# Optimization experiments

Measured on AMD Instinct MI355X. Metric: run time of the kernel, lower is better.

Reference implementation:

```python
import jax, jax.numpy as jnp
import numpy as np

# dims: batch, seq, vocab, hidden, layers, heads, head_dim, intermediate
B, S, V, Hd, L, H, D, I = 2, 1024, 32000, 1024, 4, 16, 64, 4096
THETA = 1e6
EPS = 1e-6
TOPK = S // 2          # sparsity_ratio = 0.5 -> keep half of the keys per head
STD = 0.02
NEG = -1e9


def _ln(x, w, b):
    m = jnp.mean(x, -1, keepdims=True)
    v = jnp.mean((x - m) ** 2, -1, keepdims=True)
    return (x - m) * jax.lax.rsqrt(v + EPS) * w + b


def _rope_tables():
    inv = 1.0 / (THETA ** (np.arange(0, D, 2, dtype=np.float32) / D))
    f = np.arange(S, dtype=np.float32)[:, None] * inv[None, :]   # [S, D/2]
    emb = np.concatenate([f, f], -1)                              # [S, D]
    return jnp.asarray(np.cos(emb)), jnp.asarray(np.sin(emb))


def _rot(x):  # rotate-half, x: [B,H,S,D]
    x1, x2 = jnp.split(x, 2, axis=-1)
    return jnp.concatenate([-x2, x1], -1)


def setup_inputs() -> dict:
    key = jax.random.key(0)
    it = iter(jax.random.split(key, 24))
    p = lambda sh: jax.random.normal(next(it), sh, jnp.float32) * STD
    return {
        "input_ids": jax.random.randint(next(it), (B, S), 0, V, jnp.int32),
        "attention_mask": jnp.ones((B, S), jnp.float32),
        "embed": p((V, Hd)),
        "ln1_w": jnp.ones((L, Hd)), "ln1_b": jnp.zeros((L, Hd)),
        "Wq": p((L, Hd, Hd)), "Wk": p((L, Hd, Hd)),
        "Wv": p((L, Hd, Hd)), "Wo": p((L, Hd, Hd)),
        "Wr": p((L, Hd, H)),
        "ln2_w": jnp.ones((L, Hd)), "ln2_b": jnp.zeros((L, Hd)),
        "W1": p((L, Hd, I)), "b1": jnp.zeros((L, I)),
        "W2": p((L, I, Hd)), "b2": jnp.zeros((L, Hd)),
        "norm_w": jnp.ones((Hd,)), "norm_b": jnp.zeros((Hd,)),
        "lm_head": p((Hd, V)),
    }


def reference(input_ids, attention_mask, embed, ln1_w, ln1_b, Wq, Wk, Wv, Wo,
              Wr, ln2_w, ln2_b, W1, b1, W2, b2, norm_w, norm_b, lm_head):
    cos, sin = _rope_tables()                                   # [S, D]
    mask_add = (1.0 - attention_mask)[:, None, None, :] * NEG   # [B,1,1,S]
    x = embed[input_ids]                                        # [B,S,Hd]
    scale = 1.0 / np.sqrt(D)

    def block(x, p):
        h = _ln(x, p["ln1_w"], p["ln1_b"])
        heads = lambda w: jnp.einsum('bse,ed->bsd', h, w).reshape(B, S, H, D).transpose(0, 2, 1, 3)
        q, k, v = heads(p["Wq"]), heads(p["Wk"]), heads(p["Wv"])  # [B,H,S,D]
        q = q * cos + _rot(q) * sin
        k = k * cos + _rot(k) * sin
        router = jnp.einsum('bse,eh->bhs', h, p["Wr"])            # [B,H,S]
        kth = jax.lax.top_k(router, TOPK)[0][..., -1:]            # [B,H,1]
        bias = jnp.where(router >= kth, jax.nn.log_sigmoid(router), NEG)[:, :, None, :]
        logits = jnp.einsum('bhsd,bhtd->bhst', q, k) * scale + bias + mask_add
        attn = jax.nn.softmax(logits, -1)
        o = jnp.einsum('bhst,bhtd->bhsd', attn, v).transpose(0, 2, 1, 3).reshape(B, S, Hd)
        x = x + jnp.einsum('bse,ed->bsd', o, p["Wo"])
        h2 = _ln(x, p["ln2_w"], p["ln2_b"])
        m = jax.nn.silu(jnp.einsum('bse,ei->bsi', h2, p["W1"]) + p["b1"])
        x = x + jnp.einsum('bsi,ie->bse', m, p["W2"]) + p["b2"]
        return x, None

    layer_params = {"ln1_w": ln1_w, "ln1_b": ln1_b, "Wq": Wq, "Wk": Wk,
                    "Wv": Wv, "Wo": Wo, "Wr": Wr, "ln2_w": ln2_w,
                    "ln2_b": ln2_b, "W1": W1, "b1": b1, "W2": W2, "b2": b2}
    x, _ = jax.lax.scan(block, x, layer_params)
    x = _ln(x, norm_w, norm_b)
    return jnp.einsum('bse,ev->bsv', x, lm_head)   # [B,S,V]
```

## Files before the change

kernel.cpp:

```cpp
#include <hip/hip_runtime.h>
#include <hip/hip_bf16.h>

#define Bdim 2
#define Sdim 1024
#define Vdim 32000
#define HDdim 1024
#define Ldim 4
#define Hdim 16
#define Ddim 64
#define Idim 4096
#define BSdim 2048

typedef __attribute__((ext_vector_type(8))) short bf16x8;
typedef __attribute__((ext_vector_type(4))) float f32x4;

__device__ __forceinline__ unsigned short f2bf(float f) {
    __hip_bfloat16 h = __float2bfloat16(f);
    return *reinterpret_cast<unsigned short*>(&h);
}

#define MFMA16(a, b, c) __builtin_amdgcn_mfma_f32_16x16x32_bf16((a), (b), (c), 0, 0, 0)

#define GLD16(gp, lp)                                                            \
    __builtin_amdgcn_global_load_lds((const __attribute__((address_space(1))) void*)(gp), \
                                     (__attribute__((address_space(3))) void*)(lp), 16, 0, 0)

template <int N>
__device__ __forceinline__ void vwait() {
    if constexpr (N == 2) asm volatile("s_waitcnt vmcnt(2)" ::: "memory");
    else if constexpr (N == 3) asm volatile("s_waitcnt vmcnt(3)" ::: "memory");
    else if constexpr (N == 4) asm volatile("s_waitcnt vmcnt(4)" ::: "memory");
    else if constexpr (N == 6) asm volatile("s_waitcnt vmcnt(6)" ::: "memory");
}

__global__ __launch_bounds__(256) void tables_kernel(float* __restrict__ cosT, float* __restrict__ sinT) {
    int i = blockIdx.x * 256 + threadIdx.x;
    int d = i & 63;
    int s = i >> 6;
    float inv = powf(1.0e6f, -((float)(2 * (d & 31))) / 64.0f);
    float f = (float)s * inv;
    cosT[i] = cosf(f);
    sinT[i] = sinf(f);
}

__global__ __launch_bounds__(256) void embed_kernel(const int* __restrict__ ids, const float* __restrict__ emb,
                                                    float* __restrict__ x) {
    int m = blockIdx.x;
    int tid = threadIdx.x;
    int id = ids[m];
    const float4* src = (const float4*)(emb + (size_t)id * HDdim);
    ((float4*)(x + (size_t)m * HDdim))[tid] = src[tid];
}

__global__ __launch_bounds__(256) void ln_kernel(const float* __restrict__ x, const float* __restrict__ w,
                                                 const float* __restrict__ bw, unsigned short* __restrict__ outH,
                                                 const float* __restrict__ Wr, float* __restrict__ routerO) {
    int m = blockIdx.x;
    int tid = threadIdx.x;
    float4 a = ((const float4*)(x + (size_t)m * HDdim))[tid];
    float s = a.x + a.y + a.z + a.w;
    #pragma unroll
    for (int o = 1; o < 64; o <<= 1) s += __shfl_xor(s, o);
    __shared__ float red[4], red2[4];
    if ((tid & 63) == 0) red[tid >> 6] = s;
    __syncthreads();
    float mean = (red[0] + red[1] + red[2] + red[3]) * (1.0f / 1024.0f);
    float dx = a.x - mean, dy = a.y - mean, dz = a.z - mean, dw = a.w - mean;
    float s2 = dx * dx + dy * dy + dz * dz + dw * dw;
    #pragma unroll
    for (int o = 1; o < 64; o <<= 1) s2 += __shfl_xor(s2, o);
    if ((tid & 63) == 0) red2[tid >> 6] = s2;
    __syncthreads();
    float var = (red2[0] + red2[1] + red2[2] + red2[3]) * (1.0f / 1024.0f);
    float rs = rsqrtf(var + 1e-6f);
    float4 wv = ((const float4*)w)[tid];
    float4 bv = ((const float4*)bw)[tid];
    float v0 = dx * rs * wv.x + bv.x;
    float v1 = dy * rs * wv.y + bv.y;
    float v2 = dz * rs * wv.z + bv.z;
    float v3 = dw * rs * wv.w + bv.w;
    short4 st = make_short4((short)f2bf(v0), (short)f2bf(v1), (short)f2bf(v2), (short)f2bf(v3));
    *(short4*)(outH + (size_t)m * HDdim + tid * 4) = st;

    if (Wr) {
        __shared__ float rbuf[256][16];
        __shared__ float pbuf[16][17];
        float part[16];
        const float* wr0 = Wr + (size_t)(tid * 4) * Hdim;
        #pragma unroll
        for (int h = 0; h < 16; h++)
            part[h] = v0 * wr0[h] + v1 * wr0[16 + h] + v2 * wr0[32 + h] + v3 * wr0[48 + h];
        #pragma unroll
        for (int h4 = 0; h4 < 4; h4++)
            *(float4*)&rbuf[tid][h4 * 4] = make_float4(part[h4 * 4], part[h4 * 4 + 1], part[h4 * 4 + 2], part[h4 * 4 + 3]);
        __syncthreads();
        {
            int h = tid & 15, g = tid >> 4;
            float sgr = 0.0f;
            #pragma unroll
            for (int i = 0; i < 16; i++) sgr += rbuf[g * 16 + i][h];
            pbuf[g][h] = sgr;
        }
        __syncthreads();
        if (tid < 16) {
            float tot = 0.0f;
            #pragma unroll
            for (int g = 0; g < 16; g++) tot += pbuf[g][tid];
            int b = m >> 10, sI = m & 1023;
            routerO[((size_t)(b * Hdim + tid)) * Sdim + sI] = tot;
        }
    }
}

__global__ __launch_bounds__(1024) void topk_kernel(const float* __restrict__ router, const float* __restrict__ amask,
                                                    float* __restrict__ biasC, int* __restrict__ idxC,
                                                    int* __restrict__ ntA) {
    int bh = blockIdx.x;
    int t = threadIdx.x;
    __shared__ float r[1024];
    __shared__ float kths;
    __shared__ int wcnt[16];
    float v = router[(size_t)bh * Sdim + t];
    r[t] = v;
    __syncthreads();
    int gt = 0, eq = 0;
    for (int j = 0; j < 1024; j++) {
        float xv = r[j];
        gt += (xv > v) ? 1 : 0;
        eq += (xv == v) ? 1 : 0;
    }
    if (gt < 512 && gt + eq >= 512) kths = v;
    biasC[(size_t)bh * Sdim + t] = -1e9f;
    idxC[(size_t)bh * Sdim + t] = 0;
    __syncthreads();
    float kth = kths;
    bool sel = (v >= kth);
    unsigned long long m = __ballot(sel);
    int wid = t >> 6, lane = t & 63;
    if (lane == 0) wcnt[wid] = __popcll(m);
    __syncthreads();
    int base = 0;
    for (int w = 0; w < wid; w++) base += wcnt[w];
    if (sel) {
        int rank = base + (int)__popcll(m & ((1ull << lane) - 1ull));
        float bias = (v >= 0.0f) ? -log1pf(expf(-v)) : (v - log1pf(expf(v)));
        int b = bh >> 4;
        bias += (1.0f - amask[b * Sdim + t]) * (-1e9f);
        biasC[(size_t)bh * Sdim + rank] = bias;
        idxC[(size_t)bh * Sdim + rank] = t;
    }
    if (t == 0) {
        int tot = 0;
        #pragma unroll
        for (int w = 0; w < 16; w++) tot += wcnt[w];
        ntA[bh] = (tot + 63) >> 6;
    }
}

__global__ __launch_bounds__(256) void tconv_kernel(const float* __restrict__ S0,
                                                    unsigned short* __restrict__ D, int K, int ldS) {
    __shared__ float t[32][33];
    int kt = blockIdx.y * 32, nt = blockIdx.x * 32;
    int r = threadIdx.x >> 3, c4 = (threadIdx.x & 7) * 4;
    float4 v = *(const float4*)(S0 + (size_t)(kt + r) * ldS + nt + c4);
    t[r][c4] = v.x; t[r][c4 + 1] = v.y; t[r][c4 + 2] = v.z; t[r][c4 + 3] = v.w;
    __syncthreads();
    short4 o = make_short4((short)f2bf(t[c4][r]), (short)f2bf(t[c4 + 1][r]),
                           (short)f2bf(t[c4 + 2][r]), (short)f2bf(t[c4 + 3][r]));
    *(short4*)(D + (size_t)(nt + r) * K + kt + c4) = o;
}

__global__ __launch_bounds__(256) void tconv_all(const float* __restrict__ Wq, const float* __restrict__ Wk,
                                                 const float* __restrict__ Wv, const float* __restrict__ Wo,
                                                 const float* __restrict__ W1, const float* __restrict__ W2,
                                                 unsigned short* __restrict__ wtsL) {
    const size_t M1 = 1u << 20;
    int bid = blockIdx.x;
    int lid = bid / 12288, sub = bid - lid * 12288;
    unsigned short* wl = wtsL + (size_t)lid * 12 * M1;
    const float* S;
    unsigned short* D;
    int K, ldS, nt, kt;
    if (sub < 4096) {
        int z = sub >> 10, t = sub & 1023;
        S = ((z == 0) ? Wq : (z == 1) ? Wk : (z == 2) ? Wv : Wo) + (size_t)lid * M1;
        D = wl + (size_t)z * M1;
        K = 1024; ldS = 1024; nt = t & 31; kt = t >> 5;
    } else if (sub < 8192) {
        int t = sub - 4096;
        S = W1 + (size_t)lid * 4 * M1; D = wl + 4 * M1;
        K = 1024; ldS = 4096; nt = t % 128; kt = t / 128;
    } else {
        int t = sub - 8192;
        S = W2 + (size_t)lid * 4 * M1; D = wl + 8 * M1;
        K = 4096; ldS = 1024; nt = t % 32; kt = t / 32;
    }
    __shared__ float tb[32][33];
    int ktb = kt * 32, ntb = nt * 32;
    int r = threadIdx.x >> 3, c4 = (threadIdx.x & 7) * 4;
    float4 v = *(const float4*)(S + (size_t)(ktb + r) * ldS + ntb + c4);
    tb[r][c4] = v.x; tb[r][c4 + 1] = v.y; tb[r][c4 + 2] = v.z; tb[r][c4 + 3] = v.w;
    __syncthreads();
    short4 o = make_short4((short)f2bf(tb[c4][r]), (short)f2bf(tb[c4 + 1][r]),
                           (short)f2bf(tb[c4 + 2][r]), (short)f2bf(tb[c4 + 3][r]));
    *(short4*)(D + (size_t)(ntb + r) * K + ktb + c4) = o;
}

__global__ __launch_bounds__(256) void vgather_kernel(const unsigned short* __restrict__ v16,
                                                      const int* __restrict__ idxC, const int* __restrict__ ntA,
                                                      unsigned short* __restrict__ vTc) {
    int jt = blockIdx.x;
    int bh = blockIdx.y;
    if (jt >= ntA[bh]) return;
    __shared__ unsigned short T[64][72];
    int tid = threadIdx.x;
    int jl = tid >> 2;
    int part = tid & 3;
    int j = jt * 64 + jl;
    int src = idxC[(size_t)bh * Sdim + j];
    const unsigned short* vr = v16 + ((size_t)bh * Sdim + src) * Ddim + part * 16;
    *(bf16x8*)&T[jl][part * 16] = *(const bf16x8*)vr;
    *(bf16x8*)&T[jl][part * 16 + 8] = *(const bf16x8*)(vr + 8);
    __syncthreads();
    int d = tid >> 2;
    int xr = (d & 7) << 3;
    unsigned short* dst = vTc + ((size_t)bh * Ddim + d) * Sdim + jt * 64;
    #pragma unroll
    for (int cc = 0; cc < 2; cc++) {
        int tb = (tid & 3) * 16 + cc * 8;
        bf16x8 o;
        #pragma unroll
        for (int i = 0; i < 8; i++) o[i] = (short)T[tb + i][d];
        *(bf16x8*)(dst + (tb ^ xr)) = o;
    }
}

template <int EPI, int BM, int BN, int WM, int WN>
__global__ __launch_bounds__(512) void gemm8p(
    const unsigned short* __restrict__ A, const unsigned short* __restrict__ Bt,
    float* __restrict__ OF, unsigned short* __restrict__ Hq, unsigned short* __restrict__ Hk,
    unsigned short* __restrict__ Hv, const float* __restrict__ bias,
    const float* __restrict__ cosT, const float* __restrict__ sinT,
    int Kc, int ldK, int ldC, int gridM, int gridN) {
    constexpr int MI = BM / WM / 16, NI = BN / WN / 16;
    constexpr int MH = MI / 2, NH = NI / 2;
    constexpr int LA = BM / 128, LB = BN / 128;
    constexpr int HA = BM / WM / 2;
    constexpr int HB = BN / WN / 2;
    constexpr int ABUF = BM * 64, BBUF = BN * 64;

    __shared__ unsigned short lds[2 * ABUF + 2 * BBUF];

    int bid = blockIdx.x;
    const int nwg = gridDim.x;
    if ((nwg & 7) == 0) bid = (bid & 7) * (nwg >> 3) + (bid >> 3);
    const int mn = gridM * gridN;
    const int ks = bid / mn;
    const int rem = bid - ks * mn;
    const int bm = (rem % gridM) * BM;
    const int bn = (rem / gridM) * BN;
    const unsigned short* Ap = A + (size_t)ks * Kc;
    const unsigned short* Bp = Bt + (size_t)ks * Kc;

    const int tid = threadIdx.x;
    const int lane = tid & 63, wid = tid >> 6;
    const int lc = lane & 15, lg = lane >> 4;
    const int wwm = wid / WN, wwn = wid % WN;

    const int srow = tid >> 3;
    const int scol = ((tid & 7) ^ (srow & 7)) * 8;
    const int ak0 = (lg * 8) ^ ((lc & 7) * 8);
    const int ak1 = (32 + lg * 8) ^ ((lc & 7) * 8);

    f32x4 acc[MI][NI];
    f32x4 zero = {0.0f, 0.0f, 0.0f, 0.0f};
    #pragma unroll
    for (int i = 0; i < MI; i++)
        #pragma unroll
        for (int j = 0; j < NI; j++) acc[i][j] = zero;

    bf16x8 a[MH][2], b0[NH][2], b1[NH][2];

    auto stage_a = [&](int half, int nbuf, int kt) {
        #pragma unroll
        for (int j = 0; j < LA; j++) {
            const int idx = j * 64 + srow;
            const int grow = (idx / HA) * (BM / WM) + half * HA + (idx % HA);
            const unsigned short* g = Ap + (size_t)(bm + grow) * ldK + kt + scol;
            GLD16(g, &lds[nbuf * ABUF + half * (ABUF / 2) + (j * 512 + tid) * 8]);
        }
    };
    auto stage_b = [&](int half, int nbuf, int kt) {
        #pragma unroll
        for (int j = 0; j < LB; j++) {
            const int idx = j * 64 + srow;
            const int grow = (idx / HB) * (BN / WN) + half * HB + (idx % HB);
            const unsigned short* g = Bp + (size_t)(bn + grow) * ldK + kt + scol;
            GLD16(g, &lds[2 * ABUF + nbuf * BBUF + half * (BBUF / 2) + (j * 512 + tid) * 8]);
        }
    };

#define DS_A(mh_, cur_)                                                                   \
    _Pragma("unroll") for (int m = 0; m < MH; m++) {                                      \
        const int ro = (cur_)*ABUF + (mh_) * (ABUF / 2) + (wwm * HA + m * 16 + lc) * 64;  \
        a[m][0] = *(const bf16x8*)&lds[ro + ak0];                                         \
        a[m][1] = *(const bf16x8*)&lds[ro + ak1];                                         \
    }
#define DS_B(bb_, nh_, cur_)                                                              \
    _Pragma("unroll") for (int n = 0; n < NH; n++) {                                      \
        const int ro = 2 * ABUF + (cur_)*BBUF + (nh_) * (BBUF / 2) + (wwn * HB + n * 16 + lc) * 64; \
        bb_[n][0] = *(const bf16x8*)&lds[ro + ak0];                                       \
        bb_[n][1] = *(const bf16x8*)&lds[ro + ak1];                                       \
    }
#define MFMA_PH(mh_, nh_, bb_)                                                            \
    __builtin_amdgcn_s_setprio(1);                                                        \
    _Pragma("unroll") for (int m = 0; m < MH; m++) _Pragma("unroll") for (int n = 0; n < NH; n++) { \
        acc[(mh_)*MH + m][(nh_)*NH + n] = MFMA16(a[m][0], bb_[n][0], acc[(mh_)*MH + m][(nh_)*NH + n]); \
        acc[(mh_)*MH + m][(nh_)*NH + n] = MFMA16(a[m][1], bb_[n][1], acc[(mh_)*MH + m][(nh_)*NH + n]); \
    }                                                                                     \
    __builtin_amdgcn_s_setprio(0);
#define BAR_PRE()                                                                         \
    __builtin_amdgcn_sched_barrier(0);                                                    \
    __builtin_amdgcn_s_barrier();
#define BAR_END()                                                                         \
    asm volatile("" ::: "memory");                                                        \
    __builtin_amdgcn_s_barrier();                                                         \
    __builtin_amdgcn_sched_barrier(0);

    stage_a(0, 0, 0);
    stage_b(0, 0, 0);
    stage_b(1, 0, 0);
    stage_a(1, 0, 0);
    vwait<LA + LB>();
    BAR_END();

    const int NT = Kc >> 6;
    for (int t = 0; t < NT; t++) {
        const int cur = t & 1, nxt = cur ^ 1;
        const int ktn = (t + 1 < NT) ? (t + 1) * 64 : t * 64;
        DS_A(0, cur);
        DS_B(b0, 0, cur);
        stage_a(0, nxt, ktn);
        BAR_PRE();
        MFMA_PH(0, 0, b0);
        vwait<2 * LA>();
        BAR_END();
        DS_B(b1, 1, cur);
        stage_b(0, nxt, ktn);
        BAR_PRE();
        MFMA_PH(0, 1, b1);
        vwait<LA + LB>();
        BAR_END();
        DS_A(1, cur);
        stage_b(1, nxt, ktn);
        BAR_PRE();
        MFMA_PH(1, 1, b1);
        BAR_END();
        stage_a(1, nxt, ktn);
        BAR_PRE();
        MFMA_PH(1, 0, b0);
        vwait<LA + LB>();
        BAR_END();
    }
    asm volatile("s_waitcnt vmcnt(0)" ::: "memory");
#undef DS_A
#undef DS_B
#undef MFMA_PH
#undef BAR_PRE
#undef BAR_END

    #pragma unroll
    for (int i = 0; i < MI; i++) {
        if (EPI == 1) {
            const int colbase = bn + wwn * (BN / WN);
            const int zc = colbase >> 10;
            unsigned short* OH = (zc == 0) ? Hq : (zc == 1) ? Hk : Hv;
            const int hcol = (colbase >> 6) & 15;
            #pragma unroll
            for (int r = 0; r < 4; r++) {
                int row = bm + wwm * (BM / WM) + i * 16 + lg * 4 + r;
                int b = row >> 10, s = row & 1023;
                size_t base = ((size_t)(b * Hdim + hcol) * Sdim + s) << 6;
                if (zc == 2) {
                    #pragma unroll
                    for (int j = 0; j < 4; j++) OH[base + j * 16 + lc] = f2bf(acc[i][j][r]);
                } else {
                    #pragma unroll
                    for (int j = 0; j < 2; j++) {
                        int d = j * 16 + lc;
                        float x1 = acc[i][j][r];
                        float x2 = acc[i][j + 2][r];
                        float c = cosT[s * 64 + d];
                        float sn = sinT[s * 64 + d];
                        OH[base + d] = f2bf(x1 * c - x2 * sn);
                        OH[base + d + 32] = f2bf(x2 * c + x1 * sn);
                    }
                }
            }
        } else {
            #pragma unroll
            for (int r = 0; r < 4; r++) {
                int row = bm + wwm * (BM / WM) + i * 16 + lg * 4 + r;
                #pragma unroll
                for (int j = 0; j < NI; j++) {
                    int col = bn + wwn * (BN / WN) + j * 16 + lc;
                    float v = acc[i][j][r];
                    if (EPI == 3) {
                        float t = v + bias[col];
                        Hq[(size_t)row * ldC + col] = f2bf(t / (1.0f + expf(-t)));
                    } else if (EPI == 6) {
                        if (ks == 0 && bias != nullptr) v += bias[col];
                        unsafeAtomicAdd(&OF[(size_t)row * ldC + col], v);
                    } else {
                        OF[(size_t)row * ldC + col] = v;
                    }
                }
            }
        }
    }
}

__global__ __launch_bounds__(256) void attn_kernel(const unsigned short* __restrict__ q16,
                                                   const unsigned short* __restrict__ k16,
                                                   const unsigned short* __restrict__ vTc,
                                                   const int* __restrict__ idxC,
                                                   const float* __restrict__ biasC,
                                                   const int* __restrict__ ntA,
                                                   unsigned short* __restrict__ o16) {
    const int qb = blockIdx.x;
    const int bh = blockIdx.y;
    const int tid = threadIdx.x;
    const int w = tid >> 6, lane = tid & 63;
    const int lg = lane >> 4, lc = lane & 15;
    const int nt = ntA[bh];

    __shared__ unsigned short Ks[2][64 * 64];
    __shared__ unsigned short Vs[2][64 * 64];
    __shared__ unsigned short Pq[4][16][72];
    __shared__ float sbAll[1024];

    {
        const float4 bv = ((const float4*)(biasC + (size_t)bh * Sdim))[tid];
        *(float4*)&sbAll[tid * 4] = bv;
    }

    const int qrow = qb * 64 + w * 16 + lc;
    const unsigned short* qbase = q16 + ((size_t)bh * Sdim + qrow) * Ddim;
    bf16x8 qf[2];
    qf[0] = *(const bf16x8*)(qbase + lg * 8);
    qf[1] = *(const bf16x8*)(qbase + 32 + lg * 8);

    const int grow = tid >> 3;
    const int gc = (tid & 7) * 8;
    const int ksw = (grow & 7) << 3;
    const unsigned short* kbase = k16 + (size_t)bh * Sdim * Ddim;
    const int* ibase = idxC + (size_t)bh * Sdim;
    const unsigned short* vbase = vTc + (size_t)bh * Ddim * Sdim;

    auto stageK = [&](int buf, int t1) {
        int s0 = ibase[t1 + grow];
        int s1 = ibase[t1 + 32 + grow];
        GLD16(kbase + (size_t)s0 * Ddim + (gc ^ ksw), &Ks[buf][tid * 8]);
        GLD16(kbase + (size_t)s1 * Ddim + (gc ^ ksw), &Ks[buf][2048 + tid * 8]);
    };

    {
        stageK(0, 0);
        const unsigned short* vg = vbase + (size_t)grow * Sdim + gc;
        GLD16(vg, &Vs[0][tid * 8]);
        GLD16(vg + 32 * Sdim, &Vs[0][2048 + tid * 8]);
    }
    __syncthreads();

    float m_i = -1e30f, l_i = 0.0f;
    f32x4 ot[4];
    f32x4 zero = {0.0f, 0.0f, 0.0f, 0.0f};
    #pragma unroll
    for (int fd = 0; fd < 4; fd++) ot[fd] = zero;

    const int sw = (lc & 7) << 3;

    for (int tt = 0; tt < nt; tt++) {
        const int cur = tt & 1;
        if (tt > 0) {
            asm volatile("s_waitcnt vmcnt(0)" ::: "memory");
            __builtin_amdgcn_sched_barrier(0);
            __builtin_amdgcn_s_barrier();
        }
        if (tt < nt - 1) {
            const int t1 = (tt + 1) * 64;
            stageK(cur ^ 1, t1);
            const unsigned short* vg = vbase + (size_t)grow * Sdim + t1 + gc;
            GLD16(vg, &Vs[cur ^ 1][tid * 8]);
            GLD16(vg + 32 * Sdim, &Vs[cur ^ 1][2048 + tid * 8]);
        }

        f32x4 sf[4];
        #pragma unroll
        for (int f = 0; f < 4; f++) {
            const int trow = f * 16 + lc;
            f32x4 a = zero;
            #pragma unroll
            for (int ks = 0; ks < 2; ks++) {
                bf16x8 kfr = *(bf16x8*)&Ks[cur][trow * 64 + ((ks * 32 + lg * 8) ^ sw)];
                a = MFMA16(kfr, qf[ks], a);
            }
            sf[f] = a;
        }
        const int t0 = tt * 64;
        float tmax = -1e30f;
        #pragma unroll
        for (int f = 0; f < 4; f++)
            #pragma unroll
            for (int j = 0; j < 4; j++) {
                float v = sf[f][j] * 0.125f + sbAll[t0 + f * 16 + lg * 4 + j];
                sf[f][j] = v;
                tmax = fmaxf(tmax, v);
            }
        tmax = fmaxf(tmax, __shfl_xor(tmax, 16));
        tmax = fmaxf(tmax, __shfl_xor(tmax, 32));
        float mnew = fmaxf(m_i, tmax);
        float alpha = expf(m_i - mnew);
        float lsum = 0.0f;
        #pragma unroll
        for (int f = 0; f < 4; f++)
            #pragma unroll
            for (int j = 0; j < 4; j++) {
                float p = expf(sf[f][j] - mnew);
                sf[f][j] = p;
                lsum += p;
            }
        lsum += __shfl_xor(lsum, 16);
        lsum += __shfl_xor(lsum, 32);
        l_i = l_i * alpha + lsum;
        m_i = mnew;
        #pragma unroll
        for (int fd = 0; fd < 4; fd++)
            #pragma unroll
            for (int j = 0; j < 4; j++) ot[fd][j] *= alpha;
        #pragma unroll
        for (int f = 0; f < 4; f++) {
            short4 ps = make_short4((short)f2bf(sf[f][0]), (short)f2bf(sf[f][1]),
                                    (short)f2bf(sf[f][2]), (short)f2bf(sf[f][3]));
            *(short4*)&Pq[w][lc][f * 16 + lg * 4] = ps;
        }
        #pragma unroll
        for (int ks = 0; ks < 2; ks++) {
            bf16x8 pf = *(bf16x8*)&Pq[w][lc][ks * 32 + lg * 8];
            #pragma unroll
            for (int fd = 0; fd < 4; fd++) {
                bf16x8 vfr = *(bf16x8*)&Vs[cur][(fd * 16 + lc) * 64 + ((ks * 32 + lg * 8) ^ sw)];
                ot[fd] = MFMA16(vfr, pf, ot[fd]);
            }
        }
    }
    asm volatile("s_waitcnt vmcnt(0)" ::: "memory");
    float rl = 1.0f / l_i;
    int b = bh >> 4, h = bh & 15;
    #pragma unroll
    for (int fd = 0; fd < 4; fd++)
        #pragma unroll
        for (int j = 0; j < 4; j++) {
            int d = fd * 16 + lg * 4 + j;
            o16[((size_t)b * Sdim + qrow) * HDdim + h * 64 + d] = f2bf(ot[fd][j] * rl);
        }
}

extern "C" void kernel_launch(void* const* d_in, const int* in_sizes, int n_in,
                              void* d_out, int out_size, void* d_ws, size_t ws_size,
                              hipStream_t stream) {
    const int* ids = (const int*)d_in[0];
    const float* amask = (const float*)d_in[1];
    const float* emb = (const float*)d_in[2];
    const float* ln1w = (const float*)d_in[3];
    const float* ln1b = (const float*)d_in[4];
    const float* Wq = (const float*)d_in[5];
    const float* Wk = (const float*)d_in[6];
    const float* Wv = (const float*)d_in[7];
    const float* Wo = (const float*)d_in[8];
    const float* Wr = (const float*)d_in[9];
    const float* ln2w = (const float*)d_in[10];
    const float* ln2b = (const float*)d_in[11];
    const float* W1 = (const float*)d_in[12];
    const float* b1 = (const float*)d_in[13];
    const float* W2 = (const float*)d_in[14];
    const float* b2 = (const float*)d_in[15];
    const float* nw = (const float*)d_in[16];
    const float* nb = (const float*)d_in[17];
    const float* lmh = (const float*)d_in[18];
    float* out = (float*)d_out;

    char* p = (char*)d_ws;
    size_t off = 0;
    auto alloc = [&](size_t bytes) -> void* {
        void* r = p + off;
        off += (bytes + 255) & ~(size_t)255;
        return r;
    };
    float* cosT = (float*)alloc((size_t)Sdim * Ddim * 4);
    float* sinT = (float*)alloc((size_t)Sdim * Ddim * 4);
    float* x = (float*)alloc((size_t)BSdim * HDdim * 4);
    unsigned short* h16 = (unsigned short*)alloc((size_t)BSdim * HDdim * 2);
    unsigned short* o16 = (unsigned short*)alloc((size_t)BSdim * HDdim * 2);
    unsigned short* m16 = (unsigned short*)alloc((size_t)BSdim * Idim * 2);
    unsigned short* q16 = (unsigned short*)alloc((size_t)Bdim * Hdim * Sdim * Ddim * 2);
    unsigned short* k16 = (unsigned short*)alloc((size_t)Bdim * Hdim * Sdim * Ddim * 2);
    unsigned short* v16 = (unsigned short*)alloc((size_t)Bdim * Hdim * Sdim * Ddim * 2);
    unsigned short* vTc = (unsigned short*)alloc((size_t)Bdim * Hdim * Sdim * Ddim * 2);
    float* router = (float*)alloc((size_t)Bdim * Hdim * Sdim * 4);
    float* biasC = (float*)alloc((size_t)Bdim * Hdim * Sdim * 4);
    int* idxC = (int*)alloc((size_t)Bdim * Hdim * Sdim * 4);
    int* ntA = (int*)alloc((size_t)Bdim * Hdim * 4);
    unsigned short* wts = (unsigned short*)alloc((size_t)Vdim * HDdim * 2);
    unsigned short* wtsL = (unsigned short*)alloc((size_t)Ldim * 12 * (1u << 20) * 2);

    const size_t M1 = 1u << 20;

    tables_kernel<<<256, 256, 0, stream>>>(cosT, sinT);
    embed_kernel<<<BSdim, 256, 0, stream>>>(ids, emb, x);
    tconv_kernel<<<dim3(1000, 32, 1), 256, 0, stream>>>(lmh, wts, HDdim, Vdim);
    tconv_all<<<Ldim * 12288, 256, 0, stream>>>(Wq, Wk, Wv, Wo, W1, W2, wtsL);

    for (int l = 0; l < Ldim; l++) {
        unsigned short* wl = wtsL + (size_t)l * 12 * M1;
        const float* Wr_l = Wr + (size_t)l * HDdim * Hdim;
        const float* b1_l = b1 + (size_t)l * Idim;
        const float* b2_l = b2 + (size_t)l * HDdim;

        ln_kernel<<<BSdim, 256, 0, stream>>>(x, ln1w + l * HDdim, ln1b + l * HDdim, h16, Wr_l, router);
        topk_kernel<<<Bdim * Hdim, 1024, 0, stream>>>(router, amask, biasC, idxC, ntA);
        gemm8p<1, 128, 128, 4, 2><<<384, 512, 0, stream>>>(h16, wl, nullptr, q16, k16, v16,
                                                           nullptr, cosT, sinT, HDdim, HDdim, 0, 16, 24);
        vgather_kernel<<<dim3(16, 32), 256, 0, stream>>>(v16, idxC, ntA, vTc);
        attn_kernel<<<dim3(16, 32), 256, 0, stream>>>(q16, k16, vTc, idxC, biasC, ntA, o16);
        gemm8p<6, 128, 128, 4, 2><<<256, 512, 0, stream>>>(o16, wl + 3 * M1, x, nullptr, nullptr, nullptr,
                                                           nullptr, nullptr, nullptr, 512, HDdim, HDdim, 16, 8);
        ln_kernel<<<BSdim, 256, 0, stream>>>(x, ln2w + l * HDdim, ln2b + l * HDdim, h16, nullptr, nullptr);
        gemm8p<3, 128, 128, 4, 2><<<512, 512, 0, stream>>>(h16, wl + 4 * M1, nullptr, m16, nullptr, nullptr,
                                                           b1_l, nullptr, nullptr, HDdim, HDdim, Idim, 16, 32);
        gemm8p<6, 128, 128, 4, 2><<<512, 512, 0, stream>>>(m16, wl + 8 * M1, x, nullptr, nullptr, nullptr,
                                                           b2_l, nullptr, nullptr, 1024, Idim, HDdim, 16, 8);
    }

    ln_kernel<<<BSdim, 256, 0, stream>>>(x, nw, nb, h16, nullptr, nullptr);
    gemm8p<5, 256, 256, 2, 4><<<1000, 512, 0, stream>>>(h16, wts, out, nullptr, nullptr, nullptr,
                                                        nullptr, nullptr, nullptr, HDdim, HDdim, Vdim, 8, 125);
}
```

Before: 1.028 ms.

## Replace split-K atomics with partial buffers reduced in LayerNorm; merge setup kernels

The split-K Wo and W2 GEMMs now write per-split partial sums to separate buffers instead of doing atomic adds into x. The following LayerNorm kernel sums those partials, adds the residual and bias, and writes x back. The embed and rope-table kernels are merged into one launch, as are the LM-head and layer-weight conversion kernels. The final LM-head GEMM is split into two launches over column halves. This removes atomic traffic and some launches, at the cost of extra partial-buffer memory and reads.

```diff
diff --git a/kernel.cpp b/kernel.cpp
--- a/kernel.cpp
+++ b/kernel.cpp
@@ -33,31 +33,47 @@
     else if constexpr (N == 6) asm volatile("s_waitcnt vmcnt(6)" ::: "memory");
 }
 
-__global__ __launch_bounds__(256) void tables_kernel(float* __restrict__ cosT, float* __restrict__ sinT) {
-    int i = blockIdx.x * 256 + threadIdx.x;
-    int d = i & 63;
-    int s = i >> 6;
-    float inv = powf(1.0e6f, -((float)(2 * (d & 31))) / 64.0f);
-    float f = (float)s * inv;
-    cosT[i] = cosf(f);
-    sinT[i] = sinf(f);
-}
-
-__global__ __launch_bounds__(256) void embed_kernel(const int* __restrict__ ids, const float* __restrict__ emb,
-                                                    float* __restrict__ x) {
-    int m = blockIdx.x;
+__global__ __launch_bounds__(256) void init_kernel(const int* __restrict__ ids, const float* __restrict__ emb,
+                                                   float* __restrict__ x, float* __restrict__ cosT,
+                                                   float* __restrict__ sinT) {
+    int bid = blockIdx.x;
     int tid = threadIdx.x;
-    int id = ids[m];
-    const float4* src = (const float4*)(emb + (size_t)id * HDdim);
-    ((float4*)(x + (size_t)m * HDdim))[tid] = src[tid];
-}
-
-__global__ __launch_bounds__(256) void ln_kernel(const float* __restrict__ x, const float* __restrict__ w,
-                                                 const float* __restrict__ bw, unsigned short* __restrict__ outH,
+    if (bid < BSdim) {
+        int id = ids[bid];
+        const float4* src = (const float4*)(emb + (size_t)id * HDdim);
+        ((float4*)(x + (size_t)bid * HDdim))[tid] = src[tid];
+    } else {
+        int i = (bid - BSdim) * 256 + tid;
+        int d = i & 63;
+        int s = i >> 6;
+        float inv = powf(1.0e6f, -((float)(2 * (d & 31))) / 64.0f);
+        float f = (float)s * inv;
+        cosT[i] = cosf(f);
+        sinT[i] = sinf(f);
+    }
+}
+
+template <int NP>
+__global__ __launch_bounds__(256) void ln_kernel(const float* __restrict__ x, float* __restrict__ xout,
+                                                 const float* __restrict__ parts, size_t pstride,
+                                                 const float* __restrict__ badd,
+                                                 const float* __restrict__ w, const float* __restrict__ bw,
+                                                 unsigned short* __restrict__ outH,
                                                  const float* __restrict__ Wr, float* __restrict__ routerO) {
     int m = blockIdx.x;
     int tid = threadIdx.x;
     float4 a = ((const float4*)(x + (size_t)m * HDdim))[tid];
+    #pragma unroll
+    for (int p = 0; p < NP; p++) {
+        float4 q = ((const float4*)(parts + p * pstride + (size_t)m * HDdim))[tid];
+        a.x += q.x; a.y += q.y; a.z += q.z; a.w += q.w;
+    }
+    if (badd) {
+        float4 bb = ((const float4*)badd)[tid];
+        a.x += bb.x; a.y += bb.y; a.z += bb.z; a.w += bb.w;
+    }
+    if (xout) ((float4*)(xout + (size_t)m * HDdim))[tid] = a;
+
     float s = a.x + a.y + a.z + a.w;
     #pragma unroll
     for (int o = 1; o < 64; o <<= 1) s += __shfl_xor(s, o);
@@ -157,43 +173,38 @@
     }
 }
 
-__global__ __launch_bounds__(256) void tconv_kernel(const float* __restrict__ S0,
-                                                    unsigned short* __restrict__ D, int K, int ldS) {
-    __shared__ float t[32][33];
-    int kt = blockIdx.y * 32, nt = blockIdx.x * 32;
-    int r = threadIdx.x >> 3, c4 = (threadIdx.x & 7) * 4;
-    float4 v = *(const float4*)(S0 + (size_t)(kt + r) * ldS + nt + c4);
-    t[r][c4] = v.x; t[r][c4 + 1] = v.y; t[r][c4 + 2] = v.z; t[r][c4 + 3] = v.w;
-    __syncthreads();
-    short4 o = make_short4((short)f2bf(t[c4][r]), (short)f2bf(t[c4 + 1][r]),
-                           (short)f2bf(t[c4 + 2][r]), (short)f2bf(t[c4 + 3][r]));
-    *(short4*)(D + (size_t)(nt + r) * K + kt + c4) = o;
-}
-
 __global__ __launch_bounds__(256) void tconv_all(const float* __restrict__ Wq, const float* __restrict__ Wk,
                                                  const float* __restrict__ Wv, const float* __restrict__ Wo,
                                                  const float* __restrict__ W1, const float* __restrict__ W2,
-                                                 unsigned short* __restrict__ wtsL) {
+                                                 const float* __restrict__ lmh,
+                                                 unsigned short* __restrict__ wtsL,
+                                                 unsigned short* __restrict__ wtsLM) {
     const size_t M1 = 1u << 20;
     int bid = blockIdx.x;
-    int lid = bid / 12288, sub = bid - lid * 12288;
-    unsigned short* wl = wtsL + (size_t)lid * 12 * M1;
     const float* S;
     unsigned short* D;
     int K, ldS, nt, kt;
-    if (sub < 4096) {
-        int z = sub >> 10, t = sub & 1023;
-        S = ((z == 0) ? Wq : (z == 1) ? Wk : (z == 2) ? Wv : Wo) + (size_t)lid * M1;
-        D = wl + (size_t)z * M1;
-        K = 1024; ldS = 1024; nt = t & 31; kt = t >> 5;
-    } else if (sub < 8192) {
-        int t = sub - 4096;
-        S = W1 + (size_t)lid * 4 * M1; D = wl + 4 * M1;
-        K = 1024; ldS = 4096; nt = t % 128; kt = t / 128;
+    if (bid < 49152) {
+        int lid = bid / 12288, sub = bid - lid * 12288;
+        unsigned short* wl = wtsL + (size_t)lid * 12 * M1;
+        if (sub < 4096) {
+            int z = sub >> 10, t = sub & 1023;
+            S = ((z == 0) ? Wq : (z == 1) ? Wk : (z == 2) ? Wv : Wo) + (size_t)lid * M1;
+            D = wl + (size_t)z * M1;
+            K = 1024; ldS = 1024; nt = t & 31; kt = t >> 5;
+        } else if (sub < 8192) {
+            int t = sub - 4096;
+            S = W1 + (size_t)lid * 4 * M1; D = wl + 4 * M1;
+            K = 1024; ldS = 4096; nt = t % 128; kt = t / 128;
+        } else {
+            int t = sub - 8192;
+            S = W2 + (size_t)lid * 4 * M1; D = wl + 8 * M1;
+            K = 4096; ldS = 1024; nt = t % 32; kt = t / 32;
+        }
     } else {
-        int t = sub - 8192;
-        S = W2 + (size_t)lid * 4 * M1; D = wl + 8 * M1;
-        K = 4096; ldS = 1024; nt = t % 32; kt = t / 32;
+        int t = bid - 49152;
+        S = lmh; D = wtsLM;
+        K = 1024; ldS = Vdim; nt = t % 1000; kt = t / 1000;
     }
     __shared__ float tb[32][33];
     int ktb = kt * 32, ntb = nt * 32;
@@ -241,7 +252,7 @@
     float* __restrict__ OF, unsigned short* __restrict__ Hq, unsigned short* __restrict__ Hk,
     unsigned short* __restrict__ Hv, const float* __restrict__ bias,
     const float* __restrict__ cosT, const float* __restrict__ sinT,
-    int Kc, int ldK, int ldC, int gridM, int gridN) {
+    int Kc, int ldK, int ldC, int gridM, int gridN, size_t ksStride) {
     constexpr int MI = BM / WM / 16, NI = BN / WN / 16;
     constexpr int MH = MI / 2, NH = NI / 2;
     constexpr int LA = BM / 128, LB = BN / 128;
@@ -398,6 +409,7 @@
                 }
             }
         } else {
+            float* OFk = OF + (size_t)ks * ksStride;
             #pragma unroll
             for (int r = 0; r < 4; r++) {
                 int row = bm + wwm * (BM / WM) + i * 16 + lg * 4 + r;
@@ -408,11 +420,8 @@
                     if (EPI == 3) {
                         float t = v + bias[col];
                         Hq[(size_t)row * ldC + col] = f2bf(t / (1.0f + expf(-t)));
-                    } else if (EPI == 6) {
-                        if (ks == 0 && bias != nullptr) v += bias[col];
-                        unsafeAtomicAdd(&OF[(size_t)row * ldC + col], v);
                     } else {
-                        OF[(size_t)row * ldC + col] = v;
+                        OFk[(size_t)row * ldC + col] = v;
                     }
                 }
             }
@@ -611,15 +620,16 @@
     float* biasC = (float*)alloc((size_t)Bdim * Hdim * Sdim * 4);
     int* idxC = (int*)alloc((size_t)Bdim * Hdim * Sdim * 4);
     int* ntA = (int*)alloc((size_t)Bdim * Hdim * 4);
+    float* po = (float*)alloc((size_t)2 * BSdim * HDdim * 4);
+    float* pw = (float*)alloc((size_t)4 * BSdim * HDdim * 4);
     unsigned short* wts = (unsigned short*)alloc((size_t)Vdim * HDdim * 2);
     unsigned short* wtsL = (unsigned short*)alloc((size_t)Ldim * 12 * (1u << 20) * 2);
 
     const size_t M1 = 1u << 20;
-
-    tables_kernel<<<256, 256, 0, stream>>>(cosT, sinT);
-    embed_kernel<<<BSdim, 256, 0, stream>>>(ids, emb, x);
-    tconv_kernel<<<dim3(1000, 32, 1), 256, 0, stream>>>(lmh, wts, HDdim, Vdim);
-    tconv_all<<<Ldim * 12288, 256, 0, stream>>>(Wq, Wk, Wv, Wo, W1, W2, wtsL);
+    const size_t PS = (size_t)BSdim * HDdim;
+
+    init_kernel<<<BSdim + 256, 256, 0, stream>>>(ids, emb, x, cosT, sinT);
+    tconv_all<<<49152 + 32000, 256, 0, stream>>>(Wq, Wk, Wv, Wo, W1, W2, lmh, wtsL, wts);
 
     for (int l = 0; l < Ldim; l++) {
         unsigned short* wl = wtsL + (size_t)l * 12 * M1;
@@ -627,22 +637,32 @@
         const float* b1_l = b1 + (size_t)l * Idim;
         const float* b2_l = b2 + (size_t)l * HDdim;
 
-        ln_kernel<<<BSdim, 256, 0, stream>>>(x, ln1w + l * HDdim, ln1b + l * HDdim, h16, Wr_l, router);
+        if (l == 0)
+            ln_kernel<0><<<BSdim, 256, 0, stream>>>(x, nullptr, nullptr, 0, nullptr,
+                                                    ln1w + l * HDdim, ln1b + l * HDdim, h16, Wr_l, router);
+        else
+            ln_kernel<4><<<BSdim, 256, 0, stream>>>(x, x, pw, PS, b2 + (size_t)(l - 1) * HDdim,
+                                                    ln1w + l * HDdim, ln1b + l * HDdim, h16, Wr_l, router);
         topk_kernel<<<Bdim * Hdim, 1024, 0, stream>>>(router, amask, biasC, idxC, ntA);
         gemm8p<1, 128, 128, 4, 2><<<384, 512, 0, stream>>>(h16, wl, nullptr, q16, k16, v16,
-                                                           nullptr, cosT, sinT, HDdim, HDdim, 0, 16, 24);
+                                                           nullptr, cosT, sinT, HDdim, HDdim, 0, 16, 24, 0);
         vgather_kernel<<<dim3(16, 32), 256, 0, stream>>>(v16, idxC, ntA, vTc);
         attn_kernel<<<dim3(16, 32), 256, 0, stream>>>(q16, k16, vTc, idxC, biasC, ntA, o16);
-        gemm8p<6, 128, 128, 4, 2><<<256, 512, 0, stream>>>(o16, wl + 3 * M1, x, nullptr, nullptr, nullptr,
-                                                           nullptr, nullptr, nullptr, 512, HDdim, HDdim, 16, 8);
-        ln_kernel<<<BSdim, 256, 0, stream>>>(x, ln2w + l * HDdim, ln2b + l * HDdim, h16, nullptr, nullptr);
+        gemm8p<5, 128, 128, 4, 2><<<256, 512, 0, stream>>>(o16, wl + 3 * M1, po, nullptr, nullptr, nullptr,
+                                                           nullptr, nullptr, nullptr, 512, HDdim, HDdim, 16, 8, PS);
+        ln_kernel<2><<<BSdim, 256, 0, stream>>>(x, x, po, PS, nullptr,
+                                                ln2w + l * HDdim, ln2b + l * HDdim, h16, nullptr, nullptr);
         gemm8p<3, 128, 128, 4, 2><<<512, 512, 0, stream>>>(h16, wl + 4 * M1, nullptr, m16, nullptr, nullptr,
-                                                           b1_l, nullptr, nullptr, HDdim, HDdim, Idim, 16, 32);
-        gemm8p<6, 128, 128, 4, 2><<<512, 512, 0, stream>>>(m16, wl + 8 * M1, x, nullptr, nullptr, nullptr,
-                                                           b2_l, nullptr, nullptr, 1024, Idim, HDdim, 16, 8);
-    }
-
-    ln_kernel<<<BSdim, 256, 0, stream>>>(x, nw, nb, h16, nullptr, nullptr);
-    gemm8p<5, 256, 256, 2, 4><<<1000, 512, 0, stream>>>(h16, wts, out, nullptr, nullptr, nullptr,
-                                                        nullptr, nullptr, nullptr, HDdim, HDdim, Vdim, 8, 125);
-}
+                                                           b1_l, nullptr, nullptr, HDdim, HDdim, Idim, 16, 32, 0);
+        gemm8p<5, 128, 128, 4, 2><<<512, 512, 0, stream>>>(m16, wl + 8 * M1, pw, nullptr, nullptr, nullptr,
+                                                           nullptr, nullptr, nullptr, 1024, Idim, HDdim, 16, 8, PS);
+    }
+
+    ln_kernel<4><<<BSdim, 256, 0, stream>>>(x, nullptr, pw, PS, b2 + (size_t)3 * HDdim,
+                                            nw, nb, h16, nullptr, nullptr);
+    gemm8p<5, 256, 256, 2, 4><<<496, 512, 0, stream>>>(h16, wts, out, nullptr, nullptr, nullptr,
+                                                       nullptr, nullptr, nullptr, HDdim, HDdim, Vdim, 8, 62, 0);
+    gemm8p<5, 256, 256, 2, 4><<<504, 512, 0, stream>>>(h16, wts + (size_t)62 * 256 * HDdim, out + 62 * 256,
+                                                       nullptr, nullptr, nullptr, nullptr, nullptr, nullptr,
+                                                       HDdim, HDdim, Vdim, 8, 63, 0);
+}
```

Result: faster. 988.9 us (-3.8%).
